# Performance work log

Hardware: AMD Instinct MI355X
Metric: run time of the kernel (lower is better)

The kernel has to match this reference:

```python
import jax, jax.numpy as jnp
import numpy as np

B, L, H, N = 256, 50, 128, 100000
NEG_MASK = -1.0e9  # value used by torch masked_fill_ on attention scores


def setup_inputs() -> dict:
    key = jax.random.key(0)
    ks = jax.random.split(key, 12)
    s = 1.0 / np.sqrt(H)
    return {
        "all_memory": jax.random.normal(ks[0], (B, L, H), jnp.float32),
        "last_memory": jax.random.normal(ks[1], (B, H), jnp.float32),
        "seq_item": jax.random.randint(ks[2], (B, L), 0, N),
        "mask": jnp.zeros((B, L), dtype=bool),
        # parameters (eval mode: dropout is identity)
        "Ue_w": jax.random.normal(ks[3], (H, H), jnp.float32) * s,
        "Ue_b": jnp.zeros((H,), jnp.float32),
        "We_w": jax.random.normal(ks[4], (H, H), jnp.float32) * s,
        "We_b": jnp.zeros((H,), jnp.float32),
        "Ve_w": jax.random.normal(ks[5], (H, 1), jnp.float32) * s,
        "Ve_b": jnp.zeros((1,), jnp.float32),
        "Wexp": jax.random.normal(ks[6], (2 * H, N), jnp.float32) * (1.0 / np.sqrt(2 * H)),
    }


def reference(all_memory, last_memory, seq_item, mask,
              Ue_w, Ue_b, We_w, We_b, Ve_w, Ve_b, Wexp):
    # Additive (Bahdanau) attention over the sequence
    a = jnp.einsum('blh,hk->blk', all_memory, Ue_w) + Ue_b          # [B,L,H]
    q = last_memory @ We_w + We_b                                    # [B,H]
    scores = jnp.squeeze(jnp.tanh(a + q[:, None, :]) @ Ve_w, -1) + Ve_b  # [B,L]
    scores = jnp.where(mask, NEG_MASK, scores)
    attn = jax.nn.softmax(scores, axis=1)                            # [B,L]
    ctx = jnp.einsum('bl,blh->bh', attn, all_memory)                 # [B,H]
    feat = jnp.concatenate([ctx, last_memory], axis=1)               # [B,2H]
    logits = feat @ Wexp                                             # [B,N]
    # explore mask: count of each item in the history (positions with item>0),
    # equivalent to bmm((seq_item>0), one_hot(seq_item)) without the dense one-hot
    valid = (seq_item > 0).astype(logits.dtype)                      # [B,L]
    counts = jnp.zeros((B, N), logits.dtype).at[
        jnp.arange(B)[:, None], seq_item].add(valid)                 # [B,N]
    logits = jnp.where(counts > 0, -jnp.inf, logits)
    return jax.nn.softmax(logits, axis=1)
```

## Files before the change

### kernel.cpp

```cpp
#include <hip/hip_runtime.h>
#include <math.h>

#define B_ 256
#define L_ 50
#define H_ 128
#define N_ 100000
#define K_ 256
#define NREP 64

typedef __attribute__((ext_vector_type(8))) short short8;
typedef __attribute__((ext_vector_type(4))) float f32x4;

__device__ inline short f2bf(float x) {
  union { float f; unsigned u; } v; v.f = x;
  unsigned r = (v.u + 0x7fff + ((v.u >> 16) & 1)) >> 16;
  return (short)r;
}
__device__ inline float bf2f(short h) {
  union { unsigned u; float f; } v; v.u = ((unsigned)(unsigned short)h) << 16;
  return v.f;
}

__global__ __launch_bounds__(256)
void attn_feat_kernel(const float* __restrict__ am, const float* __restrict__ lm,
    const float* __restrict__ Ue_w, const float* __restrict__ Ue_b,
    const float* __restrict__ We_w, const float* __restrict__ We_b,
    const float* __restrict__ Ve_w, const float* __restrict__ Ve_b,
    const unsigned char* __restrict__ mask,
    short* __restrict__ feat_hi, short* __restrict__ feat_lo,
    float* __restrict__ sums_rep)
{
  const int b = blockIdx.x;
  const int t = threadIdx.x;
  __shared__ float UeS[H_ * H_];
  __shared__ float amS[L_][H_];
  __shared__ float lmS[H_], qS[H_];
  __shared__ float attnS[64];
  __shared__ float redW[4][32];

  if (t < 64) sums_rep[b * 64 + t] = 0.0f;

  for (int i = t; i < H_ * H_ / 4; i += 256)
    ((float4*)UeS)[i] = ((const float4*)Ue_w)[i];
  for (int i = t; i < L_ * H_ / 4; i += 256)
    ((float4*)amS)[i] = ((const float4*)(am + (size_t)b * L_ * H_))[i];
  if (t < H_) lmS[t] = lm[b * H_ + t];
  __syncthreads();

  if (t < H_) {
    float q = We_b[t];
    #pragma unroll 8
    for (int h = 0; h < H_; ++h) q += lmS[h] * We_w[h * H_ + t];
    qS[t] = q;
  }
  __syncthreads();

  const int k = t & 127, half = t >> 7, wv = t >> 6, lk = t & 63;
  const float ve  = Ve_w[k];
  const float ueb = Ue_b[k];
  const float veb = Ve_b[0];
  for (int li = 0; li < 25; ++li) {
    const int l = half * 25 + li;
    float a = ueb;
    #pragma unroll 8
    for (int h = 0; h < H_; ++h) a = fmaf(amS[l][h], UeS[h * H_ + k], a);
    float v = tanhf(a + qS[k]) * ve;
    #pragma unroll
    for (int off = 32; off > 0; off >>= 1) v += __shfl_down(v, off, 64);
    if (lk == 0) redW[wv][li] = v;
  }
  __syncthreads();
  if (t < 50) {
    const int hf = t / 25, li = t - hf * 25;
    attnS[t] = redW[hf * 2][li] + redW[hf * 2 + 1][li] + veb;
  }
  __syncthreads();

  if (t < 64) {
    float s = (t < L_) ? attnS[t] : -3.0e38f;
    if (t < L_ && mask[b * L_ + t]) s = -1.0e9f;
    float m = s;
    #pragma unroll
    for (int off = 32; off > 0; off >>= 1) m = fmaxf(m, __shfl_xor(m, off));
    float e = (t < L_) ? __expf(s - m) : 0.0f;
    float tot = e;
    #pragma unroll
    for (int off = 32; off > 0; off >>= 1) tot += __shfl_xor(tot, off);
    if (t < L_) attnS[t] = e / tot;
  }
  __syncthreads();

  if (t < H_) {
    float c = 0.0f;
    #pragma unroll
    for (int l = 0; l < L_; ++l) c = fmaf(attnS[l], amS[l][t], c);
    short h1 = f2bf(c);
    feat_hi[b * K_ + t] = h1;
    feat_lo[b * K_ + t] = f2bf(c - bf2f(h1));
    float lv = lmS[t];
    short h2 = f2bf(lv);
    feat_hi[b * K_ + H_ + t] = h2;
    feat_lo[b * K_ + H_ + t] = f2bf(lv - bf2f(h2));
  }
}

#define TNW 64
#define WAVES 8
#define TNB (TNW * WAVES)
#define MBR 64
#define NBX ((N_ + TNB - 1) / TNB)

__global__ __launch_bounds__(512, 2)
void logits_mfma_kernel(const short* __restrict__ feat_hi, const short* __restrict__ feat_lo,
                        const float* __restrict__ Wexp, float* __restrict__ out,
                        float* __restrict__ sums_rep)
{
  __shared__ __align__(16) short fhS[MBR * K_];
  __shared__ __align__(16) short flS[MBR * K_];

  const int t = threadIdx.x;
  const int w = t >> 6, lane = t & 63, ln = lane & 15, quad = lane >> 4;
  const int m0 = blockIdx.y * MBR;
  const int n0w = blockIdx.x * TNB + w * TNW;
  const bool tail = (n0w + TNW > N_);

  int coff[4]; float cmask[4];
  #pragma unroll
  for (int nt = 0; nt < 4; ++nt) {
    const int c = n0w + nt * 16 + ln;
    cmask[nt] = (c < N_) ? 1.0f : 0.0f;
    coff[nt] = (c < N_) ? c : (N_ - 1);
  }

  float wreg[2][32];

  #define LOADW(bi, s_)                                                        \
    do {                                                                       \
      const float* gp = Wexp + (size_t)((s_) * 32 + quad * 8) * N_;            \
      _Pragma("unroll")                                                        \
      for (int nt = 0; nt < 4; ++nt)                                           \
        _Pragma("unroll")                                                      \
        for (int j = 0; j < 8; ++j)                                            \
          wreg[bi][nt * 8 + j] = gp[(size_t)j * N_ + coff[nt]];                \
    } while (0)

  LOADW(0, 0);

  {
    const int slot = t & 31;
    const int row0 = t >> 5;
    #pragma unroll
    for (int i = 0; i < 4; ++i) {
      const int row = row0 + i * 16;
      const short8 vh = *(const short8*)(feat_hi + (size_t)(m0 + row) * K_ + slot * 8);
      const short8 vl = *(const short8*)(feat_lo + (size_t)(m0 + row) * K_ + slot * 8);
      const int byte = (row * 512 + slot * 16) ^ ((row & 7) << 4);
      *(short8*)((char*)fhS + byte) = vh;
      *(short8*)((char*)flS + byte) = vl;
    }
  }
  __syncthreads();

  f32x4 acc[4][4];
  #pragma unroll
  for (int i = 0; i < 4; ++i)
    #pragma unroll
    for (int j = 0; j < 4; ++j) acc[i][j] = (f32x4)(0.0f);

  #pragma unroll
  for (int s = 0; s < 8; ++s) {
    if (s < 7) LOADW((s + 1) & 1, s + 1);
    const int bi = s & 1;

    short8 bh[4], bl[4];
    #pragma unroll
    for (int nt = 0; nt < 4; ++nt) {
      #pragma unroll
      for (int j = 0; j < 8; ++j) {
        float f = wreg[bi][nt * 8 + j];
        if (tail) f *= cmask[nt];
        union { float f; unsigned u; } v_; v_.f = f;
        union { unsigned u; float f; } h_; h_.u = v_.u & 0xffff0000u;
        bh[nt][j] = (short)(v_.u >> 16);
        bl[nt][j] = f2bf(f - h_.f);
      }
    }

    short8 ah[4], al[4];
    #pragma unroll
    for (int mt = 0; mt < 4; ++mt) {
      const int byte = ((mt * 16 + ln) * 512 + s * 64 + quad * 16) ^ ((ln & 7) << 4);
      ah[mt] = *(const short8*)((const char*)fhS + byte);
      al[mt] = *(const short8*)((const char*)flS + byte);
    }

    #pragma unroll
    for (int mt = 0; mt < 4; ++mt)
      #pragma unroll
      for (int nt = 0; nt < 4; ++nt) {
        acc[mt][nt] = __builtin_amdgcn_mfma_f32_16x16x32_bf16(ah[mt], bh[nt], acc[mt][nt], 0, 0, 0);
        acc[mt][nt] = __builtin_amdgcn_mfma_f32_16x16x32_bf16(ah[mt], bl[nt], acc[mt][nt], 0, 0, 0);
        acc[mt][nt] = __builtin_amdgcn_mfma_f32_16x16x32_bf16(al[mt], bh[nt], acc[mt][nt], 0, 0, 0);
      }
  }

  float rs[4][4];
  #pragma unroll
  for (int mt = 0; mt < 4; ++mt)
    #pragma unroll
    for (int r_ = 0; r_ < 4; ++r_) rs[mt][r_] = 0.0f;

  #pragma unroll
  for (int mt = 0; mt < 4; ++mt) {
    #pragma unroll
    for (int nt = 0; nt < 4; ++nt) {
      const int col = n0w + nt * 16 + ln;
      #pragma unroll
      for (int r_ = 0; r_ < 4; ++r_) {
        const int row = m0 + mt * 16 + quad * 4 + r_;
        const float e = __expf(acc[mt][nt][r_]);
        if (col < N_) {
          out[(size_t)row * N_ + col] = e;
          rs[mt][r_] += e;
        }
      }
    }
  }
  #pragma unroll
  for (int off = 8; off > 0; off >>= 1)
    #pragma unroll
    for (int mt = 0; mt < 4; ++mt)
      #pragma unroll
      for (int r_ = 0; r_ < 4; ++r_) rs[mt][r_] += __shfl_xor(rs[mt][r_], off, 64);

  const int my_mt = ln >> 2, my_r = ln & 3;
  const float v0_ = (my_r == 0) ? rs[0][0] : (my_r == 1) ? rs[0][1] : (my_r == 2) ? rs[0][2] : rs[0][3];
  const float v1_ = (my_r == 0) ? rs[1][0] : (my_r == 1) ? rs[1][1] : (my_r == 2) ? rs[1][2] : rs[1][3];
  const float v2_ = (my_r == 0) ? rs[2][0] : (my_r == 1) ? rs[2][1] : (my_r == 2) ? rs[2][2] : rs[2][3];
  const float v3_ = (my_r == 0) ? rs[3][0] : (my_r == 1) ? rs[3][1] : (my_r == 2) ? rs[3][2] : rs[3][3];
  const float myv = (my_mt == 0) ? v0_ : (my_mt == 1) ? v1_ : (my_mt == 2) ? v2_ : v3_;
  const int myrow = m0 + my_mt * 16 + quad * 4 + my_r;
  atomicAdd(&sums_rep[(size_t)(blockIdx.x & (NREP - 1)) * 256 + myrow], myv);
}

__global__ __launch_bounds__(256)
void reduce_sums_kernel(const float* __restrict__ sums_rep, float* __restrict__ sums)
{
  const int b = threadIdx.x;
  float s = 0.0f;
  #pragma unroll
  for (int r = 0; r < NREP; ++r) s += sums_rep[r * 256 + b];
  sums[b] = s;
}

__global__ __launch_bounds__(256)
void mask_kernel(const int* __restrict__ seq, float* __restrict__ out, float* __restrict__ sums)
{
  int idx = blockIdx.x * 256 + threadIdx.x;
  if (idx >= B_ * L_) return;
  int b = idx / L_;
  int item = seq[idx];
  if (item > 0) {
    float old = atomicExch(&out[(size_t)b * N_ + item], 0.0f);
    if (old != 0.0f) atomicAdd(&sums[b], -old);
  }
}

#define NV4 (N_ / 4)
__global__ __launch_bounds__(256)
void norm_kernel(float* __restrict__ out, const float* __restrict__ sums)
{
  const int b = blockIdx.y;
  const float inv = 1.0f / sums[b];
  float4* row = (float4*)(out + (size_t)b * N_);
  const int i0 = blockIdx.x * (256 * 4) + threadIdx.x;
  #pragma unroll
  for (int u = 0; u < 4; ++u) {
    const int i = i0 + u * 256;
    if (i < NV4) {
      float4 v = row[i];
      v.x *= inv; v.y *= inv; v.z *= inv; v.w *= inv;
      row[i] = v;
    }
  }
}

extern "C" void kernel_launch(void* const* d_in, const int* in_sizes, int n_in,
                              void* d_out, int out_size, void* d_ws, size_t ws_size,
                              hipStream_t stream)
{
  const float* am   = (const float*)d_in[0];
  const float* lm   = (const float*)d_in[1];
  const int*   seq  = (const int*)d_in[2];
  const unsigned char* mask = (const unsigned char*)d_in[3];
  const float* Ue_w = (const float*)d_in[4];
  const float* Ue_b = (const float*)d_in[5];
  const float* We_w = (const float*)d_in[6];
  const float* We_b = (const float*)d_in[7];
  const float* Ve_w = (const float*)d_in[8];
  const float* Ve_b = (const float*)d_in[9];
  const float* Wexp = (const float*)d_in[10];
  float* out = (float*)d_out;

  short* feat_hi  = (short*)d_ws;
  short* feat_lo  = feat_hi + B_ * K_;
  float* sums_rep = (float*)(feat_lo + B_ * K_);
  float* sums     = sums_rep + NREP * 256;

  attn_feat_kernel<<<B_, 256, 0, stream>>>(am, lm, Ue_w, Ue_b, We_w, We_b,
                                           Ve_w, Ve_b, mask, feat_hi, feat_lo, sums_rep);
  dim3 gB(NBX, B_ / MBR);
  logits_mfma_kernel<<<gB, 512, 0, stream>>>(feat_hi, feat_lo, Wexp, out, sums_rep);
  reduce_sums_kernel<<<1, 256, 0, stream>>>(sums_rep, sums);
  mask_kernel<<<(B_ * L_ + 255) / 256, 256, 0, stream>>>(seq, out, sums);
  dim3 gN((NV4 + 256 * 4 - 1) / (256 * 4), B_);
  norm_kernel<<<gN, 256, 0, stream>>>(out, sums);
}
```

Measured before the change: 365.8 us.

## Swizzle logits block order for XCD L2 reuse and fuse reduce+mask kernels

The logits GEMM grid becomes 1D with a remapped block index. Blocks that share the same Wexp column tile but cover different batch-row groups are spaced 8 apart, so under round-robin XCD dispatch they should land on the same XCD and share Wexp reads in its L2 instead of each fetching from HBM. The separate replica-sum reduction and explore-mask kernels are merged into one per-row kernel that subtracts the masked probabilities with a wave reduction rather than global atomics, which saves a launch. The remap hardcodes the grid dimensions and relies on an assumed dispatch order.

Measured after the change: 344.2 us. 5.9% less time.

```diff
diff --git a/kernel.cpp b/kernel.cpp
--- a/kernel.cpp
+++ b/kernel.cpp
@@ -109,6 +109,7 @@
 #define TNB (TNW * WAVES)
 #define MBR 64
 #define NBX ((N_ + TNB - 1) / TNB)
+#define GRIDB (NBX * 4)
 
 __global__ __launch_bounds__(512, 2)
 void logits_mfma_kernel(const short* __restrict__ feat_hi, const short* __restrict__ feat_lo,
@@ -120,8 +121,14 @@
 
   const int t = threadIdx.x;
   const int w = t >> 6, lane = t & 63, ln = lane & 15, quad = lane >> 4;
-  const int m0 = blockIdx.y * MBR;
-  const int n0w = blockIdx.x * TNB + w * TNW;
+
+  const int bid = blockIdx.x;
+  int x, y;
+  if (bid < 768) { x = (bid >> 5) * 8 + (bid & 7); y = (bid >> 3) & 3; }
+  else           { const int r = bid - 768; x = 192 + (r >> 2); y = r & 3; }
+
+  const int m0 = y * MBR;
+  const int n0w = x * TNB + w * TNW;
   const bool tail = (n0w + TNW > N_);
 
   int coff[4]; float cmask[4];
@@ -240,30 +247,30 @@
   const float v3_ = (my_r == 0) ? rs[3][0] : (my_r == 1) ? rs[3][1] : (my_r == 2) ? rs[3][2] : rs[3][3];
   const float myv = (my_mt == 0) ? v0_ : (my_mt == 1) ? v1_ : (my_mt == 2) ? v2_ : v3_;
   const int myrow = m0 + my_mt * 16 + quad * 4 + my_r;
-  atomicAdd(&sums_rep[(size_t)(blockIdx.x & (NREP - 1)) * 256 + myrow], myv);
-}
-
-__global__ __launch_bounds__(256)
-void reduce_sums_kernel(const float* __restrict__ sums_rep, float* __restrict__ sums)
-{
-  const int b = threadIdx.x;
-  float s = 0.0f;
-  #pragma unroll
-  for (int r = 0; r < NREP; ++r) s += sums_rep[r * 256 + b];
-  sums[b] = s;
-}
-
-__global__ __launch_bounds__(256)
-void mask_kernel(const int* __restrict__ seq, float* __restrict__ out, float* __restrict__ sums)
-{
-  int idx = blockIdx.x * 256 + threadIdx.x;
-  if (idx >= B_ * L_) return;
-  int b = idx / L_;
-  int item = seq[idx];
-  if (item > 0) {
-    float old = atomicExch(&out[(size_t)b * N_ + item], 0.0f);
-    if (old != 0.0f) atomicAdd(&sums[b], -old);
-  }
+  atomicAdd(&sums_rep[(size_t)(x & (NREP - 1)) * 256 + myrow], myv);
+}
+
+__global__ __launch_bounds__(64)
+void reduce_mask_kernel(const float* __restrict__ sums_rep, const int* __restrict__ seq,
+                        float* __restrict__ out, float* __restrict__ sums)
+{
+  const int b = blockIdx.x, t = threadIdx.x;
+  float s = sums_rep[(size_t)t * 256 + b];
+  #pragma unroll
+  for (int off = 32; off > 0; off >>= 1) s += __shfl_down(s, off, 64);
+
+  float sub = 0.0f;
+  if (t < L_) {
+    const int item = seq[b * L_ + t];
+    if (item > 0) {
+      const float old = atomicExch(&out[(size_t)b * N_ + item], 0.0f);
+      sub = old;
+    }
+  }
+  #pragma unroll
+  for (int off = 32; off > 0; off >>= 1) sub += __shfl_down(sub, off, 64);
+
+  if (t == 0) sums[b] = s - sub;
 }
 
 #define NV4 (N_ / 4)
@@ -309,10 +316,8 @@
 
   attn_feat_kernel<<<B_, 256, 0, stream>>>(am, lm, Ue_w, Ue_b, We_w, We_b,
                                            Ve_w, Ve_b, mask, feat_hi, feat_lo, sums_rep);
-  dim3 gB(NBX, B_ / MBR);
-  logits_mfma_kernel<<<gB, 512, 0, stream>>>(feat_hi, feat_lo, Wexp, out, sums_rep);
-  reduce_sums_kernel<<<1, 256, 0, stream>>>(sums_rep, sums);
-  mask_kernel<<<(B_ * L_ + 255) / 256, 256, 0, stream>>>(seq, out, sums);
+  logits_mfma_kernel<<<GRIDB, 512, 0, stream>>>(feat_hi, feat_lo, Wexp, out, sums_rep);
+  reduce_mask_kernel<<<B_, 64, 0, stream>>>(sums_rep, seq, out, sums);
   dim3 gN((NV4 + 256 * 4 - 1) / (256 * 4), B_);
   norm_kernel<<<gN, 256, 0, stream>>>(out, sums);
 }
```
